# Kernel tuning notes

Measured on AMD Instinct MI355X. Metric: run time of the kernel, lower is better.

## Reference

```python
import jax, jax.numpy as jnp
import numpy as np

B, S, E, H = 2, 2048, 1024, 16
D = E // H  # head_dim = 64


def setup_inputs() -> dict:
    key = jax.random.key(0)
    ks = jax.random.split(key, 11)
    s = 1.0 / np.sqrt(E)
    return {
        "query": jax.random.normal(ks[0], (B, S, E), jnp.float32),
        "key":   jax.random.normal(ks[1], (B, S, E), jnp.float32),
        "value": jax.random.normal(ks[2], (B, S, E), jnp.float32),
        "q_w": jax.random.uniform(ks[3], (E, E), jnp.float32, -s, s),
        "q_b": jax.random.uniform(ks[4], (E,), jnp.float32, -s, s),
        "k_w": jax.random.uniform(ks[5], (E, E), jnp.float32, -s, s),
        "k_b": jax.random.uniform(ks[6], (E,), jnp.float32, -s, s),
        "v_w": jax.random.uniform(ks[7], (E, E), jnp.float32, -s, s),
        "v_b": jax.random.uniform(ks[8], (E,), jnp.float32, -s, s),
        "o_w": jax.random.uniform(ks[9], (E, E), jnp.float32, -s, s),
        "o_b": jax.random.uniform(ks[10], (E,), jnp.float32, -s, s),
    }


def reference(query, key, value, q_w, q_b, k_w, k_b, v_w, v_b, o_w, o_b):
    b, sq, _ = query.shape
    sk = key.shape[1]
    # linear projections (torch Linear: x @ W.T + b)
    Q = (query @ q_w.T + q_b).reshape(b, sq, H, D).transpose(0, 2, 1, 3)  # b h sq d
    K = (key   @ k_w.T + k_b).reshape(b, sk, H, D).transpose(0, 2, 1, 3)
    V = (value @ v_w.T + v_b).reshape(b, sk, H, D).transpose(0, 2, 1, 3)
    scores = jnp.einsum("bhqd,bhkd->bhqk", Q, K) / jnp.sqrt(jnp.float32(D))
    attn = jax.nn.softmax(scores, axis=-1)
    out = jnp.einsum("bhqk,bhkd->bhqd", attn, V)  # b h sq d
    out = out.transpose(0, 2, 1, 3).reshape(b, sq, E)
    return out @ o_w.T + o_b
```

## Files before the change

### kernel.cpp

```cpp
#include <hip/hip_runtime.h>
#include <stdint.h>

typedef __bf16 bf16x8 __attribute__((ext_vector_type(8)));
typedef short short8 __attribute__((ext_vector_type(8)));
typedef float f32x4 __attribute__((ext_vector_type(4)));
typedef float f32x16 __attribute__((ext_vector_type(16)));
typedef unsigned short u16;
typedef unsigned int u32;

#define MROWS 4096
#define EDIM  1024
#define SQ    2048
#define DH    64

#if __has_builtin(__builtin_amdgcn_exp2f)
#define EXP2(x) __builtin_amdgcn_exp2f(x)
#else
#define EXP2(x) exp2f(x)
#endif

__device__ __forceinline__ u16 f2bf(float f) {
  unsigned u = __builtin_bit_cast(unsigned, f);
  return (u16)((u + 0x7FFFu + ((u >> 16) & 1u)) >> 16);
}

__device__ __forceinline__ u32 cvtpk_bf16(float lo, float hi) {
  u32 r;
  asm("v_cvt_pk_bf16_f32 %0, %1, %2" : "=v"(r) : "v"(lo), "v"(hi));
  return r;
}
__device__ __forceinline__ void swap32(u32& a, u32& b) {
  asm("v_permlane32_swap_b32 %0, %1" : "+v"(a), "+v"(b));
}

__global__ __launch_bounds__(256) void cvt7_kernel(
    const float* __restrict__ s0, const float* __restrict__ s1,
    const float* __restrict__ s2, const float* __restrict__ s3,
    const float* __restrict__ s4, const float* __restrict__ s5,
    const float* __restrict__ s6,
    u16* __restrict__ d0, u16* __restrict__ d1, u16* __restrict__ d2,
    u16* __restrict__ d3, u16* __restrict__ d4, u16* __restrict__ d5,
    u16* __restrict__ d6, int nact, int nw) {
  const float* s; u16* d; int n;
  switch (blockIdx.y) {
    case 0: s = s0; d = d0; n = nact; break;
    case 1: s = s1; d = d1; n = nact; break;
    case 2: s = s2; d = d2; n = nact; break;
    case 3: s = s3; d = d3; n = nw; break;
    case 4: s = s4; d = d4; n = nw; break;
    case 5: s = s5; d = d5; n = nw; break;
    default: s = s6; d = d6; n = nw; break;
  }
  int i = (blockIdx.x * 256 + threadIdx.x) * 8;
  if (i >= n) return;
  float4 a = *(const float4*)(s + i);
  float4 b = *(const float4*)(s + i + 4);
  short8 r;
  r[0] = (short)f2bf(a.x); r[1] = (short)f2bf(a.y);
  r[2] = (short)f2bf(a.z); r[3] = (short)f2bf(a.w);
  r[4] = (short)f2bf(b.x); r[5] = (short)f2bf(b.y);
  r[6] = (short)f2bf(b.z); r[7] = (short)f2bf(b.w);
  *(short8*)(d + i) = r;
}

template <int OUT_F32>
__device__ __forceinline__ void gemm_core(
    const u16* __restrict__ A, const u16* __restrict__ W,
    const float* __restrict__ bias, void* __restrict__ C,
    int m0, int n0, u16* As, u16* Bs) {
  const int tid = threadIdx.x, lane = tid & 63, w = tid >> 6;
  const int r = lane & 15, g = lane >> 4;
  const int wr = w >> 1, wc = w & 1;
  f32x4 acc[4][4] = {};

  for (int kt = 0; kt < 32; ++kt) {
    const int k0 = kt * 32;
    __syncthreads();
#pragma unroll
    for (int i = 0; i < 2; ++i) {
      int c = i * 256 + tid;
      int row = c >> 2, ko = (c & 3) * 8;
      __builtin_amdgcn_global_load_lds(
          (const __attribute__((address_space(1))) void*)(A + (size_t)(m0 + row) * EDIM + k0 + ko),
          (__attribute__((address_space(3))) void*)(As + (i * 256 + w * 64) * 8), 16, 0, 0);
      __builtin_amdgcn_global_load_lds(
          (const __attribute__((address_space(1))) void*)(W + (size_t)(n0 + row) * EDIM + k0 + ko),
          (__attribute__((address_space(3))) void*)(Bs + (i * 256 + w * 64) * 8), 16, 0, 0);
    }
    __syncthreads();
    bf16x8 af[4], bfv[4];
#pragma unroll
    for (int i = 0; i < 4; ++i) {
      af[i]  = *(const bf16x8*)&As[(wr * 64 + i * 16 + r) * 32 + g * 8];
      bfv[i] = *(const bf16x8*)&Bs[(wc * 64 + i * 16 + r) * 32 + g * 8];
    }
#pragma unroll
    for (int mi = 0; mi < 4; ++mi)
#pragma unroll
      for (int ni = 0; ni < 4; ++ni)
        acc[mi][ni] = __builtin_amdgcn_mfma_f32_16x16x32_bf16(af[mi], bfv[ni], acc[mi][ni], 0, 0, 0);
  }
#pragma unroll
  for (int ni = 0; ni < 4; ++ni) {
    const int col = n0 + wc * 64 + ni * 16 + r;
    const float bv = bias[col];
#pragma unroll
    for (int mi = 0; mi < 4; ++mi) {
#pragma unroll
      for (int rr = 0; rr < 4; ++rr) {
        const int rowm = m0 + wr * 64 + mi * 16 + g * 4 + rr;
        float v = acc[mi][ni][rr] + bv;
        if (OUT_F32) ((float*)C)[(size_t)rowm * EDIM + col] = v;
        else ((u16*)C)[(size_t)rowm * EDIM + col] = f2bf(v);
      }
    }
  }
}

__global__ __launch_bounds__(256) void gemm_qkv(
    const u16* __restrict__ X0, const u16* __restrict__ X1, const u16* __restrict__ X2,
    const u16* __restrict__ W0, const u16* __restrict__ W1, const u16* __restrict__ W2,
    const float* __restrict__ b0, const float* __restrict__ b1, const float* __restrict__ b2,
    u16* __restrict__ C0, u16* __restrict__ C1, u16* __restrict__ C2) {
  __shared__ u16 As[128 * 32];
  __shared__ u16 Bs[128 * 32];
  const u16 *A, *W; const float* bias; u16* C;
  switch (blockIdx.z) {
    case 0: A = X0; W = W0; bias = b0; C = C0; break;
    case 1: A = X1; W = W1; bias = b1; C = C1; break;
    default: A = X2; W = W2; bias = b2; C = C2; break;
  }
  gemm_core<0>(A, W, bias, C, blockIdx.y * 128, blockIdx.x * 128, As, Bs);
}

__global__ __launch_bounds__(256) void gemm_oproj(
    const u16* __restrict__ A, const u16* __restrict__ W,
    const float* __restrict__ bias, float* __restrict__ C) {
  __shared__ u16 As[128 * 32];
  __shared__ u16 Bs[128 * 32];
  gemm_core<1>(A, W, bias, C, blockIdx.y * 128, blockIdx.x * 128, As, Bs);
}

__device__ __forceinline__ void k_stage(const u16* __restrict__ Kg, int kt, int tid,
                                        int w, u16* kb) {
#pragma unroll
  for (int ri = 0; ri < 2; ++ri) {
    int idx = ri * 256 + tid, row = idx >> 3, sl = idx & 7;
    __builtin_amdgcn_global_load_lds(
        (const __attribute__((address_space(1))) void*)(
            Kg + (size_t)(kt * 64 + row) * EDIM + ((sl ^ (row & 7)) * 8)),
        (__attribute__((address_space(3))) void*)(kb + (ri * 256 + w * 64) * 8), 16, 0, 0);
  }
}

__device__ __forceinline__ void v_issue(const u16* __restrict__ Vg, int kt, int tid,
                                        u32* vdw) {
  const int vd0 = (tid & 31) * 2, kvc = tid >> 5;
#pragma unroll
  for (int j = 0; j < 8; ++j)
    vdw[j] = *(const u32*)(Vg + (size_t)(kt * 64 + kvc * 8 + j) * EDIM + vd0);
}

__device__ __forceinline__ void v_write(u16* vt, int tid, const u32* vdw) {
  const int vd0 = (tid & 31) * 2, kvc = tid >> 5;
  union { u32 u[4]; short8 s; } lo8, hi8;
#pragma unroll
  for (int i = 0; i < 4; ++i) {
    lo8.u[i] = (vdw[2 * i] & 0xFFFFu) | (vdw[2 * i + 1] << 16);
    hi8.u[i] = (vdw[2 * i] >> 16) | (vdw[2 * i + 1] & 0xFFFF0000u);
  }
  const int sl = kvc ^ (vd0 & 7);
  *(short8*)&vt[vd0 * 64 + sl * 8] = lo8.s;
  *(short8*)&vt[(vd0 + 1) * 64 + (sl ^ 1) * 8] = hi8.s;
}

__global__ __launch_bounds__(256) void attn2_kernel(
    const u16* __restrict__ Q, const u16* __restrict__ K,
    const u16* __restrict__ V, u16* __restrict__ O) {
  __shared__ __align__(16) u16 KB[2][64 * 64];
  __shared__ __align__(16) u16 VT[2][64 * 64];
  const int tid = threadIdx.x, lane = tid & 63, w = tid >> 6;
  const int lq = lane & 31, hi = lane >> 5;
  const int bid = blockIdx.x;
  const int b2 = (bid & 7) * 64 + (bid >> 3);
  const int qb = b2 & 15, bh = b2 >> 4;
  const int b = bh >> 4, h = bh & 15;
  const u16* Qg = Q + (size_t)b * SQ * EDIM + h * DH;
  const u16* Kg = K + (size_t)b * SQ * EDIM + h * DH;
  const u16* Vg = V + (size_t)b * SQ * EDIM + h * DH;
  const int q0 = qb * 128 + w * 32;
  const float CE = 0.18033688011112042f;
  const float THR = 8.0f;

  bf16x8 qf[4];
#pragma unroll
  for (int f = 0; f < 4; ++f)
    qf[f] = *(const bf16x8*)(Qg + (size_t)(q0 + lq) * EDIM + f * 16 + hi * 8);

  const int swz = (lq & 7) << 4;
  int colA[4];
#pragma unroll
  for (int f = 0; f < 4; ++f) colA[f] = ((f * 32 + hi * 16) ^ swz) >> 1;

  f32x16 accO[2] = {};
  float m = -3e38f, l = 0.f;

  u32 vdw[8];
  k_stage(Kg, 0, tid, w, KB[0]);
  v_issue(Vg, 0, tid, vdw);
  v_write(VT[0], tid, vdw);
  __syncthreads();

  for (int kt = 0; kt < 32; ++kt) {
    const int cur = kt & 1;
    if (kt < 31) {
      k_stage(Kg, kt + 1, tid, w, KB[cur ^ 1]);
      v_issue(Vg, kt + 1, tid, vdw);
    }

    f32x16 st[2] = {};
    __builtin_amdgcn_s_setprio(1);
#pragma unroll
    for (int t = 0; t < 2; ++t)
#pragma unroll
      for (int f = 0; f < 4; ++f) {
        const bf16x8 ka = *(const bf16x8*)&KB[cur][(t * 32 + lq) * 64 + colA[f]];
        st[t] = __builtin_amdgcn_mfma_f32_32x32x16_bf16(ka, qf[f], st[t], 0, 0, 0);
      }
    __builtin_amdgcn_s_setprio(0);

    float vm = fmaxf(st[0][0], st[0][1]);
#pragma unroll
    for (int t = 0; t < 2; ++t)
#pragma unroll
      for (int rr = (t == 0 ? 2 : 0); rr < 16; ++rr) vm = fmaxf(vm, st[t][rr]);
    vm = fmaxf(vm, __shfl_xor(vm, 32));
    if (!__all(vm <= m + THR)) {
      const float mn = fmaxf(m, vm);
      const float scl = EXP2((m - mn) * CE);
      m = mn;
      l *= scl;
#pragma unroll
      for (int dt = 0; dt < 2; ++dt)
#pragma unroll
        for (int rr = 0; rr < 16; ++rr) accO[dt][rr] *= scl;
    }
    const float mc = m * CE;
    float ts = 0.f;
#pragma unroll
    for (int t = 0; t < 2; ++t)
#pragma unroll
      for (int rr = 0; rr < 16; ++rr) {
        float pv = EXP2(st[t][rr] * CE - mc);
        st[t][rr] = pv;
        ts += pv;
      }
    ts += __shfl_xor(ts, 32);
    l += ts;

    bf16x8 pb[4];
#pragma unroll
    for (int t = 0; t < 2; ++t)
#pragma unroll
      for (int kh = 0; kh < 2; ++kh) {
        const int rb = kh * 8;
        u32 a0 = cvtpk_bf16(st[t][rb + 0], st[t][rb + 1]);
        u32 b0 = cvtpk_bf16(st[t][rb + 4], st[t][rb + 5]);
        swap32(a0, b0);
        u32 a1 = cvtpk_bf16(st[t][rb + 2], st[t][rb + 3]);
        u32 b1 = cvtpk_bf16(st[t][rb + 6], st[t][rb + 7]);
        swap32(a1, b1);
        union { u32 u[4]; bf16x8 v; } pu;
        pu.u[0] = a0; pu.u[1] = a1; pu.u[2] = b0; pu.u[3] = b1;
        pb[t * 2 + kh] = pu.v;
      }

    __builtin_amdgcn_s_setprio(1);
#pragma unroll
    for (int dt = 0; dt < 2; ++dt)
#pragma unroll
      for (int ks = 0; ks < 4; ++ks) {
        const bf16x8 va = *(const bf16x8*)&VT[cur][(dt * 32 + lq) * 64 + colA[ks]];
        accO[dt] = __builtin_amdgcn_mfma_f32_32x32x16_bf16(va, pb[ks], accO[dt], 0, 0, 0);
      }
    __builtin_amdgcn_s_setprio(0);

    if (kt < 31) v_write(VT[cur ^ 1], tid, vdw);
    __syncthreads();
  }

  const float rinv = 1.0f / l;
  u16* Ost = (u16*)KB;
#pragma unroll
  for (int dt = 0; dt < 2; ++dt)
#pragma unroll
    for (int rr = 0; rr < 16; ++rr) {
      const int d = dt * 32 + (rr & 3) + 8 * (rr >> 2) + 4 * hi;
      Ost[w * 2048 + lq * 64 + (d ^ ((lq & 7) << 3))] = f2bf(accO[dt][rr] * rinv);
    }
  __syncthreads();
#pragma unroll
  for (int ri = 0; ri < 4; ++ri) {
    const int idx = ri * 256 + tid;
    const int w2 = idx >> 8, q = (idx >> 3) & 31, c = idx & 7;
    short8 o = *(const short8*)&Ost[w2 * 2048 + q * 64 + ((c ^ (q & 7)) * 8)];
    *(short8*)(O + (size_t)(b * SQ + qb * 128 + w2 * 32 + q) * EDIM + h * DH + c * 8) = o;
  }
}

extern "C" void kernel_launch(void* const* d_in, const int* in_sizes, int n_in,
                              void* d_out, int out_size, void* d_ws, size_t ws_size,
                              hipStream_t stream) {
  (void)in_sizes; (void)n_in; (void)out_size; (void)ws_size;
  const float* query = (const float*)d_in[0];
  const float* key   = (const float*)d_in[1];
  const float* value = (const float*)d_in[2];
  const float* q_w = (const float*)d_in[3];
  const float* q_b = (const float*)d_in[4];
  const float* k_w = (const float*)d_in[5];
  const float* k_b = (const float*)d_in[6];
  const float* v_w = (const float*)d_in[7];
  const float* v_b = (const float*)d_in[8];
  const float* o_w = (const float*)d_in[9];
  const float* o_b = (const float*)d_in[10];

  u16* ws = (u16*)d_ws;
  const size_t NX = (size_t)MROWS * EDIM;
  const size_t NW = (size_t)EDIM * EDIM;
  u16* Xq = ws;
  u16* Xk = Xq + NX;
  u16* Xv = Xk + NX;
  u16* Wq = Xv + NX;
  u16* Wk = Wq + NW;
  u16* Wv = Wk + NW;
  u16* Wo = Wv + NW;
  u16* Qp = Wo + NW;
  u16* Kp = Qp + NX;
  u16* Vp = Kp + NX;
  u16* At = Xq;

  cvt7_kernel<<<dim3((int)(NX / 8 / 256), 7), 256, 0, stream>>>(
      query, key, value, q_w, k_w, v_w, o_w,
      Xq, Xk, Xv, Wq, Wk, Wv, Wo, (int)NX, (int)NW);

  gemm_qkv<<<dim3(8, 32, 3), 256, 0, stream>>>(
      Xq, Xk, Xv, Wq, Wk, Wv, q_b, k_b, v_b, Qp, Kp, Vp);

  attn2_kernel<<<512, 256, 0, stream>>>(Qp, Kp, Vp, At);

  gemm_oproj<<<dim3(8, 32), 256, 0, stream>>>(At, Wo, o_b, (float*)d_out);
}
```

Before: 138.8 us.

## Software-pipeline QK^T of next tile with softmax and PV of current tile

Restructures the attention loop so each iteration computes QK^T for tile T while running softmax and PV for tile T-1. Score tiles ping-pong between two register sets, and the V buffer grows to three LDS slots so the V tile consumed one step late is not overwritten. The goal is to let exp and convert VALU work overlap with independent MFMA work inside a wave instead of running back to back. In exchange it raises register pressure, with another 32 live floats for scores, and adds a prologue and epilogue.

```diff
diff --git a/kernel.cpp b/kernel.cpp
--- a/kernel.cpp
+++ b/kernel.cpp
@@ -174,11 +174,90 @@
   *(short8*)&vt[(vd0 + 1) * 64 + (sl ^ 1) * 8] = hi8.s;
 }
 
+#define CE_CONST 0.18033688011112042f
+
+__device__ __forceinline__ void qk_step(f32x16 (&st)[2], const u16* kb,
+                                        const bf16x8 (&qf)[4], const int (&colA)[4],
+                                        int lq) {
+  __builtin_amdgcn_s_setprio(1);
+#pragma unroll
+  for (int t = 0; t < 2; ++t) {
+    f32x16 z = {};
+#pragma unroll
+    for (int f = 0; f < 4; ++f) {
+      const bf16x8 ka = *(const bf16x8*)&kb[(t * 32 + lq) * 64 + colA[f]];
+      z = __builtin_amdgcn_mfma_f32_32x32x16_bf16(ka, qf[f], z, 0, 0, 0);
+    }
+    st[t] = z;
+  }
+  __builtin_amdgcn_s_setprio(0);
+}
+
+__device__ __forceinline__ void softmax_pb(f32x16 (&st)[2], float& m, float& l,
+                                           f32x16 (&accO)[2], bf16x8 (&pb)[4]) {
+  float vm = fmaxf(st[0][0], st[0][1]);
+#pragma unroll
+  for (int t = 0; t < 2; ++t)
+#pragma unroll
+    for (int rr = (t == 0 ? 2 : 0); rr < 16; ++rr) vm = fmaxf(vm, st[t][rr]);
+  vm = fmaxf(vm, __shfl_xor(vm, 32));
+  if (!__all(vm <= m + 8.0f)) {
+    const float mn = fmaxf(m, vm);
+    const float scl = EXP2((m - mn) * CE_CONST);
+    m = mn;
+    l *= scl;
+#pragma unroll
+    for (int dt = 0; dt < 2; ++dt)
+#pragma unroll
+      for (int rr = 0; rr < 16; ++rr) accO[dt][rr] *= scl;
+  }
+  const float mc = m * CE_CONST;
+  float ts = 0.f;
+#pragma unroll
+  for (int t = 0; t < 2; ++t)
+#pragma unroll
+    for (int rr = 0; rr < 16; ++rr) {
+      float pv = EXP2(st[t][rr] * CE_CONST - mc);
+      st[t][rr] = pv;
+      ts += pv;
+    }
+  ts += __shfl_xor(ts, 32);
+  l += ts;
+#pragma unroll
+  for (int t = 0; t < 2; ++t)
+#pragma unroll
+    for (int kh = 0; kh < 2; ++kh) {
+      const int rb = kh * 8;
+      u32 a0 = cvtpk_bf16(st[t][rb + 0], st[t][rb + 1]);
+      u32 b0 = cvtpk_bf16(st[t][rb + 4], st[t][rb + 5]);
+      swap32(a0, b0);
+      u32 a1 = cvtpk_bf16(st[t][rb + 2], st[t][rb + 3]);
+      u32 b1 = cvtpk_bf16(st[t][rb + 6], st[t][rb + 7]);
+      swap32(a1, b1);
+      union { u32 u[4]; bf16x8 v; } pu;
+      pu.u[0] = a0; pu.u[1] = a1; pu.u[2] = b0; pu.u[3] = b1;
+      pb[t * 2 + kh] = pu.v;
+    }
+}
+
+__device__ __forceinline__ void pv_step(f32x16 (&accO)[2], const bf16x8 (&pb)[4],
+                                        const u16* vt, const int (&colA)[4], int lq) {
+  __builtin_amdgcn_s_setprio(1);
+#pragma unroll
+  for (int dt = 0; dt < 2; ++dt)
+#pragma unroll
+    for (int ks = 0; ks < 4; ++ks) {
+      const bf16x8 va = *(const bf16x8*)&vt[(dt * 32 + lq) * 64 + colA[ks]];
+      accO[dt] = __builtin_amdgcn_mfma_f32_32x32x16_bf16(va, pb[ks], accO[dt], 0, 0, 0);
+    }
+  __builtin_amdgcn_s_setprio(0);
+}
+
 __global__ __launch_bounds__(256) void attn2_kernel(
     const u16* __restrict__ Q, const u16* __restrict__ K,
     const u16* __restrict__ V, u16* __restrict__ O) {
   __shared__ __align__(16) u16 KB[2][64 * 64];
-  __shared__ __align__(16) u16 VT[2][64 * 64];
+  __shared__ __align__(16) u16 VT[3][64 * 64];
   const int tid = threadIdx.x, lane = tid & 63, w = tid >> 6;
   const int lq = lane & 31, hi = lane >> 5;
   const int bid = blockIdx.x;
@@ -189,8 +268,6 @@
   const u16* Kg = K + (size_t)b * SQ * EDIM + h * DH;
   const u16* Vg = V + (size_t)b * SQ * EDIM + h * DH;
   const int q0 = qb * 128 + w * 32;
-  const float CE = 0.18033688011112042f;
-  const float THR = 8.0f;
 
   bf16x8 qf[4];
 #pragma unroll
@@ -203,91 +280,41 @@
   for (int f = 0; f < 4; ++f) colA[f] = ((f * 32 + hi * 16) ^ swz) >> 1;
 
   f32x16 accO[2] = {};
+  f32x16 stA[2], stB[2];
+  bf16x8 pb[4];
   float m = -3e38f, l = 0.f;
-
   u32 vdw[8];
+
   k_stage(Kg, 0, tid, w, KB[0]);
   v_issue(Vg, 0, tid, vdw);
   v_write(VT[0], tid, vdw);
   __syncthreads();
-
-  for (int kt = 0; kt < 32; ++kt) {
-    const int cur = kt & 1;
-    if (kt < 31) {
-      k_stage(Kg, kt + 1, tid, w, KB[cur ^ 1]);
-      v_issue(Vg, kt + 1, tid, vdw);
-    }
-
-    f32x16 st[2] = {};
-    __builtin_amdgcn_s_setprio(1);
-#pragma unroll
-    for (int t = 0; t < 2; ++t)
-#pragma unroll
-      for (int f = 0; f < 4; ++f) {
-        const bf16x8 ka = *(const bf16x8*)&KB[cur][(t * 32 + lq) * 64 + colA[f]];
-        st[t] = __builtin_amdgcn_mfma_f32_32x32x16_bf16(ka, qf[f], st[t], 0, 0, 0);
-      }
-    __builtin_amdgcn_s_setprio(0);
-
-    float vm = fmaxf(st[0][0], st[0][1]);
-#pragma unroll
-    for (int t = 0; t < 2; ++t)
-#pragma unroll
-      for (int rr = (t == 0 ? 2 : 0); rr < 16; ++rr) vm = fmaxf(vm, st[t][rr]);
-    vm = fmaxf(vm, __shfl_xor(vm, 32));
-    if (!__all(vm <= m + THR)) {
-      const float mn = fmaxf(m, vm);
-      const float scl = EXP2((m - mn) * CE);
-      m = mn;
-      l *= scl;
-#pragma unroll
-      for (int dt = 0; dt < 2; ++dt)
-#pragma unroll
-        for (int rr = 0; rr < 16; ++rr) accO[dt][rr] *= scl;
-    }
-    const float mc = m * CE;
-    float ts = 0.f;
-#pragma unroll
-    for (int t = 0; t < 2; ++t)
-#pragma unroll
-      for (int rr = 0; rr < 16; ++rr) {
-        float pv = EXP2(st[t][rr] * CE - mc);
-        st[t][rr] = pv;
-        ts += pv;
-      }
-    ts += __shfl_xor(ts, 32);
-    l += ts;
-
-    bf16x8 pb[4];
-#pragma unroll
-    for (int t = 0; t < 2; ++t)
-#pragma unroll
-      for (int kh = 0; kh < 2; ++kh) {
-        const int rb = kh * 8;
-        u32 a0 = cvtpk_bf16(st[t][rb + 0], st[t][rb + 1]);
-        u32 b0 = cvtpk_bf16(st[t][rb + 4], st[t][rb + 5]);
-        swap32(a0, b0);
-        u32 a1 = cvtpk_bf16(st[t][rb + 2], st[t][rb + 3]);
-        u32 b1 = cvtpk_bf16(st[t][rb + 6], st[t][rb + 7]);
-        swap32(a1, b1);
-        union { u32 u[4]; bf16x8 v; } pu;
-        pu.u[0] = a0; pu.u[1] = a1; pu.u[2] = b0; pu.u[3] = b1;
-        pb[t * 2 + kh] = pu.v;
-      }
-
-    __builtin_amdgcn_s_setprio(1);
-#pragma unroll
-    for (int dt = 0; dt < 2; ++dt)
-#pragma unroll
-      for (int ks = 0; ks < 4; ++ks) {
-        const bf16x8 va = *(const bf16x8*)&VT[cur][(dt * 32 + lq) * 64 + colA[ks]];
-        accO[dt] = __builtin_amdgcn_mfma_f32_32x32x16_bf16(va, pb[ks], accO[dt], 0, 0, 0);
-      }
-    __builtin_amdgcn_s_setprio(0);
-
-    if (kt < 31) v_write(VT[cur ^ 1], tid, vdw);
-    __syncthreads();
-  }
+  k_stage(Kg, 1, tid, w, KB[1]);
+  v_issue(Vg, 1, tid, vdw);
+  qk_step(stA, KB[0], qf, colA, lq);
+  v_write(VT[1], tid, vdw);
+  __syncthreads();
+
+#define ATTN_BODY(T, SP, SN)                                                  \
+  {                                                                           \
+    if ((T) < 31) { k_stage(Kg, (T) + 1, tid, w, KB[((T) + 1) & 1]);          \
+                    v_issue(Vg, (T) + 1, tid, vdw); }                         \
+    qk_step(SN, KB[(T) & 1], qf, colA, lq);                                   \
+    softmax_pb(SP, m, l, accO, pb);                                           \
+    pv_step(accO, pb, VT[((T) - 1) % 3], colA, lq);                           \
+    if ((T) < 31) v_write(VT[((T) + 1) % 3], tid, vdw);                       \
+    __syncthreads();                                                          \
+  }
+
+  for (int t = 1; t < 31; t += 2) {
+    ATTN_BODY(t, stA, stB);
+    ATTN_BODY(t + 1, stB, stA);
+  }
+  ATTN_BODY(31, stA, stB);
+#undef ATTN_BODY
+
+  softmax_pb(stB, m, l, accO, pb);
+  pv_step(accO, pb, VT[31 % 3], colA, lq);
 
   const float rinv = 1.0f / l;
   u16* Ost = (u16*)KB;
```

Result: no change. 137.1 us (-1.2%).
